# Kernel optimization log

Hardware: AMD Instinct MI355X
Metric: run time of the kernel (lower is better)

Reference implementation:

```python
import jax, jax.numpy as jnp
import numpy as np

F_IN = 10000
M = 3
CARD = 5
LOG_2PI = float(np.log(2.0 * np.pi))


def _normal_logprob(x, means, stds):
    # x: [N, F, 1]; means/stds: [1, F, M] -> [N, F, M]
    z = (x - means) / stds
    return -0.5 * (z * z) - jnp.log(stds) - 0.5 * LOG_2PI


def _sum_layer(x, w):
    # x: [N, F, Cin]; w: [F, Cin, Cout] -> [N, F, Cout]
    logw = jax.nn.log_softmax(w, axis=1)
    return jax.scipy.special.logsumexp(x[:, :, :, None] + logw[None], axis=2)


def _product_layer(x, card):
    # log-domain product = segmented sum over blocks of `card` features
    n, f, c = x.shape
    return x.reshape(n, f // card, card, c).sum(axis=2)


def setup_inputs() -> dict:
    key = jax.random.key(0)
    ks = jax.random.split(key, 9)
    x = jax.random.normal(ks[0], (4096, F_IN), dtype=jnp.float32)
    means = jax.random.normal(ks[1], (1, F_IN, M), dtype=jnp.float32)
    stds = jax.random.uniform(ks[2], (1, F_IN, M), dtype=jnp.float32, minval=0.5, maxval=1.5)
    w1 = jax.random.normal(ks[3], (F_IN, M, 1), dtype=jnp.float32)
    w2 = jax.random.normal(ks[4], (F_IN // 5, 1, 1), dtype=jnp.float32)
    w3 = jax.random.normal(ks[5], (F_IN // 25, 1, 1), dtype=jnp.float32)
    w4 = jax.random.normal(ks[6], (F_IN // 125, 1, 1), dtype=jnp.float32)
    w5 = jax.random.normal(ks[7], (F_IN // 625, 1, 1), dtype=jnp.float32)
    rand_idxs = jax.random.permutation(ks[8], F_IN).astype(jnp.int32)
    return {"x": x, "means": means, "stds": stds, "w1": w1, "w2": w2,
            "w3": w3, "w4": w4, "w5": w5, "rand_idxs": rand_idxs}


def reference(x, means, stds, w1, w2, w3, w4, w5, rand_idxs):
    # scope permutation gather
    xp = x[:, rand_idxs]                          # [N, F]
    y = _normal_logprob(xp[:, :, None], means, stds)  # [N, F, M]
    y = _sum_layer(y, w1)                          # [N, F, 1]
    y = _product_layer(y, CARD)                    # [N, F/5, 1]
    y = _sum_layer(y, w2)
    y = _product_layer(y, CARD)                    # [N, F/25, 1]
    y = _sum_layer(y, w3)
    y = _product_layer(y, CARD)                    # [N, F/125, 1]
    y = _sum_layer(y, w4)
    y = _product_layer(y, CARD)                    # [N, F/625, 1]
    y = _sum_layer(y, w5)
    y = _product_layer(y, F_IN // 5 ** 4)          # [N, 1, 1]
    return y
```

## Files before the change

kernel.cpp:

```cpp
#include <hip/hip_runtime.h>
#include <math.h>

#define F_IN 10000
#define NROWS 4096
#define NCHUNK 40
#define CGROUPS 8
#define ROWS_PER_WAVE 4

__global__ void spn_prep_kernel(const float* __restrict__ means,
                                const float* __restrict__ stds,
                                const float* __restrict__ w1,
                                const int* __restrict__ rand_idxs,
                                float* __restrict__ ws,
                                float* __restrict__ out) {
    int f = blockIdx.x * blockDim.x + threadIdx.x;
    if (f < NROWS) out[f] = 0.0f;
    if (f >= F_IN) return;

    int j = rand_idxs[f];

    float wa = w1[f * 3 + 0];
    float wb = w1[f * 3 + 1];
    float wc = w1[f * 3 + 2];
    float wm = fmaxf(fmaxf(wa, wb), wc);
    float lse = wm + __logf(__expf(wa - wm) + __expf(wb - wm) + __expf(wc - wm));

    const float INV_SQRT2 = 0.70710678118654752440f;
    const float HALF_LOG_2PI = 0.91893853320467274178f;

#pragma unroll
    for (int m = 0; m < 3; m++) {
        float w  = w1[f * 3 + m] - lse;
        float sd = stds[f * 3 + m];
        float mu = means[f * 3 + m];
        float a  = INV_SQRT2 / sd;
        float b  = -mu * a;
        float c  = w - __logf(sd) - HALF_LOG_2PI;
        ws[(0 + m) * F_IN + j] = a;
        ws[(3 + m) * F_IN + j] = b;
        ws[(6 + m) * F_IN + j] = c;
    }
}

__device__ __forceinline__ void col_term(float xv,
                                         float a0, float b0, float c0,
                                         float a1, float b1, float c1,
                                         float a2, float b2, float c2,
                                         float& mx_out, float& s_out) {
    float u0 = fmaf(xv, a0, b0);
    float u1 = fmaf(xv, a1, b1);
    float u2 = fmaf(xv, a2, b2);
    float v0 = fmaf(-u0, u0, c0);
    float v1 = fmaf(-u1, u1, c1);
    float v2 = fmaf(-u2, u2, c2);
    float mx = fmaxf(fmaxf(v0, v1), v2);
    float me = __builtin_amdgcn_fmed3f(v0, v1, v2);
    float mn = fminf(fminf(v0, v1), v2);
    float s  = 1.0f + __expf(me - mx) + __expf(mn - mx);
    mx_out = mx;
    s_out  = s;
}

__global__ __launch_bounds__(256) void spn_main_kernel(const float* __restrict__ x,
                                                       const float* __restrict__ ws,
                                                       float* __restrict__ out) {
    const int wave = threadIdx.x >> 6;
    const int lane = threadIdx.x & 63;
    const int rb   = blockIdx.x >> 3;
    const int cg   = blockIdx.x & 7;
    const int row0 = rb * (ROWS_PER_WAVE * 4) + wave * ROWS_PER_WAVE;

    float accm[ROWS_PER_WAVE];
    float prod[ROWS_PER_WAVE];
#pragma unroll
    for (int r = 0; r < ROWS_PER_WAVE; r++) { accm[r] = 0.0f; prod[r] = 1.0f; }

    const float* xr[ROWS_PER_WAVE];
#pragma unroll
    for (int r = 0; r < ROWS_PER_WAVE; r++) xr[r] = x + (size_t)(row0 + r) * F_IN;

    float4 xv[ROWS_PER_WAVE];
    {
        int jc = cg * 256 + lane * 4;
#pragma unroll
        for (int r = 0; r < ROWS_PER_WAVE; r++)
            xv[r] = *(const float4*)(xr[r] + jc);
    }

#pragma unroll
    for (int it = 0; it < 5; ++it) {
        const int c = cg + it * 8;
        const int jcur = c * 256 + lane * 4;
        const bool vcur = (jcur < F_IN);
        const int q = vcur ? (jcur >> 2) : 0;

        const float4 A0 = ((const float4*)(ws + 0 * F_IN))[q];
        const float4 A1 = ((const float4*)(ws + 1 * F_IN))[q];
        const float4 A2 = ((const float4*)(ws + 2 * F_IN))[q];
        const float4 B0 = ((const float4*)(ws + 3 * F_IN))[q];
        const float4 B1 = ((const float4*)(ws + 4 * F_IN))[q];
        const float4 B2 = ((const float4*)(ws + 5 * F_IN))[q];
        const float4 C0 = ((const float4*)(ws + 6 * F_IN))[q];
        const float4 C1 = ((const float4*)(ws + 7 * F_IN))[q];
        const float4 C2 = ((const float4*)(ws + 8 * F_IN))[q];

        float4 xn[ROWS_PER_WAVE];
        if (it < 4) {
            int jn = (c + 8) * 256 + lane * 4;
            int jnc = (jn < F_IN) ? jn : 0;
#pragma unroll
            for (int r = 0; r < ROWS_PER_WAVE; r++)
                xn[r] = *(const float4*)(xr[r] + jnc);
        }

#pragma unroll
        for (int r = 0; r < ROWS_PER_WAVE; r++) {
            float m0, s0, m1, s1, m2, s2, m3, s3;
            col_term(xv[r].x, A0.x, B0.x, C0.x, A1.x, B1.x, C1.x, A2.x, B2.x, C2.x, m0, s0);
            col_term(xv[r].y, A0.y, B0.y, C0.y, A1.y, B1.y, C1.y, A2.y, B2.y, C2.y, m1, s1);
            col_term(xv[r].z, A0.z, B0.z, C0.z, A1.z, B1.z, C1.z, A2.z, B2.z, C2.z, m2, s2);
            col_term(xv[r].w, A0.w, B0.w, C0.w, A1.w, B1.w, C1.w, A2.w, B2.w, C2.w, m3, s3);

            float smx = (m0 + m1) + (m2 + m3);
            float sp  = (s0 * s1) * (s2 * s3);
            accm[r] += vcur ? smx : 0.0f;
            prod[r] *= vcur ? sp : 1.0f;
        }

        if (it < 4) {
#pragma unroll
            for (int r = 0; r < ROWS_PER_WAVE; r++) xv[r] = xn[r];
        }
    }

#pragma unroll
    for (int r = 0; r < ROWS_PER_WAVE; r++) {
        float part = accm[r] + __logf(prod[r]);
#pragma unroll
        for (int off = 32; off > 0; off >>= 1)
            part += __shfl_xor(part, off, 64);
        if (lane == 0)
            atomicAdd(&out[row0 + r], part);
    }
}

extern "C" void kernel_launch(void* const* d_in, const int* in_sizes, int n_in,
                              void* d_out, int out_size, void* d_ws, size_t ws_size,
                              hipStream_t stream) {
    const float* x         = (const float*)d_in[0];
    const float* means     = (const float*)d_in[1];
    const float* stds      = (const float*)d_in[2];
    const float* w1        = (const float*)d_in[3];
    const int*   rand_idxs = (const int*)d_in[8];

    float* out = (float*)d_out;
    float* ws  = (float*)d_ws;

    spn_prep_kernel<<<(F_IN + 255) / 256, 256, 0, stream>>>(means, stds, w1, rand_idxs, ws, out);

    spn_main_kernel<<<256 * CGROUPS, 256, 0, stream>>>(x, ws, out);
}
```

Measured before the change: 247.4 us.

## Stage per-column coefficients in LDS and use nontemporal loads for x

```diff
diff --git a/kernel.cpp b/kernel.cpp
--- a/kernel.cpp
+++ b/kernel.cpp
@@ -3,9 +3,18 @@
 
 #define F_IN 10000
 #define NROWS 4096
-#define NCHUNK 40
 #define CGROUPS 8
-#define ROWS_PER_WAVE 4
+#define CH_PER_CG 5
+#define BLK 512
+#define RPW 4
+#define PASSES 2
+#define ROWBLOCKS 64
+
+typedef float v4f __attribute__((ext_vector_type(4)));
+
+__device__ __forceinline__ v4f ntload4(const float* p) {
+    return __builtin_nontemporal_load((const v4f*)p);
+}
 
 __global__ void spn_prep_kernel(const float* __restrict__ means,
                                 const float* __restrict__ stds,
@@ -61,86 +70,101 @@
     s_out  = s;
 }
 
-__global__ __launch_bounds__(256) void spn_main_kernel(const float* __restrict__ x,
+__global__ __launch_bounds__(BLK) void spn_main_kernel(const float* __restrict__ x,
                                                        const float* __restrict__ ws,
                                                        float* __restrict__ out) {
-    const int wave = threadIdx.x >> 6;
-    const int lane = threadIdx.x & 63;
+    __shared__ v4f ldsbuf[CH_PER_CG * 9 * 64];
+
+    const int tid  = threadIdx.x;
+    const int wave = tid >> 6;
+    const int lane = tid & 63;
     const int rb   = blockIdx.x >> 3;
     const int cg   = blockIdx.x & 7;
-    const int row0 = rb * (ROWS_PER_WAVE * 4) + wave * ROWS_PER_WAVE;
 
-    float accm[ROWS_PER_WAVE];
-    float prod[ROWS_PER_WAVE];
+    const v4f* wsv = (const v4f*)ws;
+    for (int i = tid; i < CH_PER_CG * 9 * 64; i += BLK) {
+        int it  = i / (9 * 64);
+        int rem = i - it * (9 * 64);
+        int a   = rem >> 6;
+        int v   = rem & 63;
+        int col = (cg + it * 8) * 256 + v * 4;
+        v4f val = (v4f)(0.0f);
+        if (col < F_IN) val = wsv[a * (F_IN / 4) + (col >> 2)];
+        ldsbuf[i] = val;
+    }
+    __syncthreads();
+
+    for (int g = 0; g < PASSES; ++g) {
+        const int row0 = rb * 64 + g * 32 + wave * RPW;
+        const float* xr0 = x + (size_t)row0 * F_IN;
+
+        float accm[RPW], prod[RPW];
 #pragma unroll
-    for (int r = 0; r < ROWS_PER_WAVE; r++) { accm[r] = 0.0f; prod[r] = 1.0f; }
+        for (int r = 0; r < RPW; r++) { accm[r] = 0.0f; prod[r] = 1.0f; }
 
-    const float* xr[ROWS_PER_WAVE];
+        v4f xv[RPW];
+        {
+            int jc = cg * 256 + lane * 4;
 #pragma unroll
-    for (int r = 0; r < ROWS_PER_WAVE; r++) xr[r] = x + (size_t)(row0 + r) * F_IN;
-
-    float4 xv[ROWS_PER_WAVE];
-    {
-        int jc = cg * 256 + lane * 4;
-#pragma unroll
-        for (int r = 0; r < ROWS_PER_WAVE; r++)
-            xv[r] = *(const float4*)(xr[r] + jc);
-    }
-
-#pragma unroll
-    for (int it = 0; it < 5; ++it) {
-        const int c = cg + it * 8;
-        const int jcur = c * 256 + lane * 4;
-        const bool vcur = (jcur < F_IN);
-        const int q = vcur ? (jcur >> 2) : 0;
-
-        const float4 A0 = ((const float4*)(ws + 0 * F_IN))[q];
-        const float4 A1 = ((const float4*)(ws + 1 * F_IN))[q];
-        const float4 A2 = ((const float4*)(ws + 2 * F_IN))[q];
-        const float4 B0 = ((const float4*)(ws + 3 * F_IN))[q];
-        const float4 B1 = ((const float4*)(ws + 4 * F_IN))[q];
-        const float4 B2 = ((const float4*)(ws + 5 * F_IN))[q];
-        const float4 C0 = ((const float4*)(ws + 6 * F_IN))[q];
-        const float4 C1 = ((const float4*)(ws + 7 * F_IN))[q];
-        const float4 C2 = ((const float4*)(ws + 8 * F_IN))[q];
-
-        float4 xn[ROWS_PER_WAVE];
-        if (it < 4) {
-            int jn = (c + 8) * 256 + lane * 4;
-            int jnc = (jn < F_IN) ? jn : 0;
-#pragma unroll
-            for (int r = 0; r < ROWS_PER_WAVE; r++)
-                xn[r] = *(const float4*)(xr[r] + jnc);
+            for (int r = 0; r < RPW; r++)
+                xv[r] = ntload4(xr0 + (size_t)r * F_IN + jc);
         }
 
 #pragma unroll
-        for (int r = 0; r < ROWS_PER_WAVE; r++) {
-            float m0, s0, m1, s1, m2, s2, m3, s3;
-            col_term(xv[r].x, A0.x, B0.x, C0.x, A1.x, B1.x, C1.x, A2.x, B2.x, C2.x, m0, s0);
-            col_term(xv[r].y, A0.y, B0.y, C0.y, A1.y, B1.y, C1.y, A2.y, B2.y, C2.y, m1, s1);
-            col_term(xv[r].z, A0.z, B0.z, C0.z, A1.z, B1.z, C1.z, A2.z, B2.z, C2.z, m2, s2);
-            col_term(xv[r].w, A0.w, B0.w, C0.w, A1.w, B1.w, C1.w, A2.w, B2.w, C2.w, m3, s3);
+        for (int it = 0; it < CH_PER_CG; ++it) {
+            const int c = cg + it * 8;
+            const int jcur = c * 256 + lane * 4;
+            const bool vcur = (jcur < F_IN);
 
-            float smx = (m0 + m1) + (m2 + m3);
-            float sp  = (s0 * s1) * (s2 * s3);
-            accm[r] += vcur ? smx : 0.0f;
-            prod[r] *= vcur ? sp : 1.0f;
+            v4f xn[RPW];
+            if (it < CH_PER_CG - 1) {
+                int jn = (c + 8) * 256 + lane * 4;
+                int jnc = (jn < F_IN) ? jn : 0;
+#pragma unroll
+                for (int r = 0; r < RPW; r++)
+                    xn[r] = ntload4(xr0 + (size_t)r * F_IN + jnc);
+            }
+
+            const v4f* Lp = ldsbuf + it * (9 * 64);
+            const v4f A0 = Lp[0 * 64 + lane];
+            const v4f A1 = Lp[1 * 64 + lane];
+            const v4f A2 = Lp[2 * 64 + lane];
+            const v4f B0 = Lp[3 * 64 + lane];
+            const v4f B1 = Lp[4 * 64 + lane];
+            const v4f B2 = Lp[5 * 64 + lane];
+            const v4f C0 = Lp[6 * 64 + lane];
+            const v4f C1 = Lp[7 * 64 + lane];
+            const v4f C2 = Lp[8 * 64 + lane];
+
+#pragma unroll
+            for (int r = 0; r < RPW; r++) {
+                float m0, s0, m1, s1, m2, s2, m3, s3;
+                col_term(xv[r].x, A0.x, B0.x, C0.x, A1.x, B1.x, C1.x, A2.x, B2.x, C2.x, m0, s0);
+                col_term(xv[r].y, A0.y, B0.y, C0.y, A1.y, B1.y, C1.y, A2.y, B2.y, C2.y, m1, s1);
+                col_term(xv[r].z, A0.z, B0.z, C0.z, A1.z, B1.z, C1.z, A2.z, B2.z, C2.z, m2, s2);
+                col_term(xv[r].w, A0.w, B0.w, C0.w, A1.w, B1.w, C1.w, A2.w, B2.w, C2.w, m3, s3);
+
+                float smx = (m0 + m1) + (m2 + m3);
+                float sp  = (s0 * s1) * (s2 * s3);
+                accm[r] += vcur ? smx : 0.0f;
+                prod[r] *= vcur ? sp : 1.0f;
+            }
+
+            if (it < CH_PER_CG - 1) {
+#pragma unroll
+                for (int r = 0; r < RPW; r++) xv[r] = xn[r];
+            }
         }
 
-        if (it < 4) {
 #pragma unroll
-            for (int r = 0; r < ROWS_PER_WAVE; r++) xv[r] = xn[r];
+        for (int r = 0; r < RPW; r++) {
+            float part = accm[r] + __logf(prod[r]);
+#pragma unroll
+            for (int off = 32; off > 0; off >>= 1)
+                part += __shfl_xor(part, off, 64);
+            if (lane == 0)
+                atomicAdd(&out[row0 + r], part);
         }
-    }
-
-#pragma unroll
-    for (int r = 0; r < ROWS_PER_WAVE; r++) {
-        float part = accm[r] + __logf(prod[r]);
-#pragma unroll
-        for (int off = 32; off > 0; off >>= 1)
-            part += __shfl_xor(part, off, 64);
-        if (lane == 0)
-            atomicAdd(&out[row0 + r], part);
     }
 }
 
@@ -158,5 +182,5 @@
 
     spn_prep_kernel<<<(F_IN + 255) / 256, 256, 0, stream>>>(means, stds, w1, rand_idxs, ws, out);
 
-    spn_main_kernel<<<256 * CGROUPS, 256, 0, stream>>>(x, ws, out);
+    spn_main_kernel<<<ROWBLOCKS * CGROUPS, BLK, 0, stream>>>(x, ws, out);
 }
```

Measured after the change: 254.0 us. 2.7% more time.
